# Kernel tuning notes

Hardware: AMD Instinct MI355X
Metric: run time of the kernel (lower is better)

## Reference

```python
import jax, jax.numpy as jnp
import numpy as np

IN, H, B = 1024, 1024, 8192


def _uniform(key, shape, stdv):
    return jax.random.uniform(key, shape, jnp.float32, -stdv, stdv)


def setup_inputs() -> dict:
    key = jax.random.key(0)
    ks = jax.random.split(key, 20)
    stdv = 1.0 / np.sqrt(H)
    inp = {
        "x": jax.random.normal(ks[0], (B, IN), jnp.float32),
        "h": jax.random.normal(ks[1], (B, H), jnp.float32),
        "c": jax.random.normal(ks[2], (B, H), jnp.float32),
        # fused input->gates weight [IN, 4H] (gate order: I, F, G, O) and bias [4H]
        "Wi": _uniform(ks[3], (IN, 4 * H), stdv),
        "bi": _uniform(ks[4], (4 * H,), stdv),
        # fused hidden->gates weight [H, 4H] and bias [4H]
        "Wh": _uniform(ks[5], (H, 4 * H), stdv),
        "bh": _uniform(ks[6], (4 * H,), stdv),
    }
    return inp


def reference(x, h, c, Wi, bi, Wh, bh):
    # Two fused GEMMs replacing the 8 separate nn.Linear calls (same math).
    gates = x @ Wi + bi + h @ Wh + bh  # [B, 4H]
    gI, gF, gG, gO = jnp.split(gates, 4, axis=-1)
    I = jax.nn.sigmoid(gI)
    F = jax.nn.sigmoid(gF)
    G = jnp.tanh(gG)   # nlF = Tanh
    O = jax.nn.sigmoid(gO)
    c_ = F * c + I * G
    h_ = O * jnp.tanh(c_)  # nlF2 = Tanh
    return (h_, c_)
```

## Files before the change

### kernel.cpp

```cpp
#include <hip/hip_runtime.h>
#include <stdint.h>

#define IN_DIM 1024
#define H_DIM  1024
#define BATCH  8192
#define KDIM   2048
#define NDIM   4096
#define BM     256
#define BN     256
#define BK     64
#define NT     (KDIM / BK)

typedef __bf16 bf16x8 __attribute__((ext_vector_type(8)));
typedef float  f32x4  __attribute__((ext_vector_type(4)));
typedef unsigned int u32;

static __device__ __forceinline__ unsigned short f2bf(float f) {
  u32 u = __builtin_bit_cast(u32, f);
  u += 0x7FFFu + ((u >> 16) & 1u);
  return (unsigned short)(u >> 16);
}

static __device__ __forceinline__ float sigm(float x) {
  return 1.0f / (1.0f + __expf(-x));
}
static __device__ __forceinline__ float tanh_fast(float x) {
  float e = __expf(-2.0f * fabsf(x));
  float t = (1.0f - e) / (1.0f + e);
  return copysignf(t, x);
}

__global__ void conv_a(const float* __restrict__ x, const float* __restrict__ h,
                       unsigned short* __restrict__ A) {
  const int total = BATCH * KDIM / 4;
  for (int i = blockIdx.x * blockDim.x + threadIdx.x; i < total;
       i += gridDim.x * blockDim.x) {
    int b = i >> 9;
    int k = (i & 511) << 2;
    const float* src = (k < IN_DIM) ? (x + (size_t)b * IN_DIM + k)
                                    : (h + (size_t)b * H_DIM + (k - IN_DIM));
    float4 v = *reinterpret_cast<const float4*>(src);
    ushort4 o;
    o.x = f2bf(v.x); o.y = f2bf(v.y); o.z = f2bf(v.z); o.w = f2bf(v.w);
    *reinterpret_cast<ushort4*>(A + (size_t)b * KDIM + k) = o;
  }
}

__global__ void conv_b(const float* __restrict__ Wi, const float* __restrict__ Wh,
                       unsigned short* __restrict__ Bt) {
  __shared__ float tile[32][33];
  int k0 = blockIdx.x * 32;
  int c0 = blockIdx.y * 32;
  int tx = threadIdx.x;
  int ty = threadIdx.y;
  const float* src = (k0 < IN_DIM) ? (Wi + (size_t)k0 * NDIM)
                                   : (Wh + (size_t)(k0 - IN_DIM) * NDIM);
  for (int i = 0; i < 4; i++) {
    int r = ty + 8 * i;
    tile[r][tx] = src[(size_t)r * NDIM + c0 + tx];
  }
  __syncthreads();
  int g = c0 >> 10;
  int ubase = c0 & 1023;
  for (int i = 0; i < 4; i++) {
    int cc = ty + 8 * i;
    int u = ubase + cc;
    int j = ((u >> 4) << 6) + (g << 4) + (u & 15);
    Bt[(size_t)j * KDIM + k0 + tx] = f2bf(tile[tx][cc]);
  }
}

__global__ void conv_bias(const float* __restrict__ bi, const float* __restrict__ bh,
                          float* __restrict__ bias) {
  int j = blockIdx.x * blockDim.x + threadIdx.x;
  if (j < NDIM) {
    int u = ((j >> 6) << 4) + (j & 15);
    int g = (j >> 4) & 3;
    int c = (g << 10) + u;
    bias[j] = bi[c] + bh[c];
  }
}

static __device__ __forceinline__ void gload_lds16(const void* g, void* l) {
  __builtin_amdgcn_global_load_lds(
      (const __attribute__((address_space(1))) u32*)g,
      (__attribute__((address_space(3))) u32*)l, 16, 0, 0);
}

#define MFMA __builtin_amdgcn_mfma_f32_16x16x32_bf16

__launch_bounds__(512, 2)
__global__ void lstm_gemm(const unsigned short* __restrict__ A,
                          const unsigned short* __restrict__ Bt,
                          const float* __restrict__ bias,
                          const float* __restrict__ Cin,
                          float* __restrict__ Hout,
                          float* __restrict__ Cout) {
  __shared__ __align__(16) char smem[131072];

  const int t  = threadIdx.x;
  const int l  = t & 63;
  const int w  = t >> 6;
  const int lane16 = l & 15;
  const int kg = l >> 4;
  const int wr = w >> 2;
  const int wc = w & 3;

  int bid = blockIdx.x;
  int swz = (bid & 7) * 64 + (bid >> 3);
  int brow = (swz >> 4) * BM;
  int bcol = (swz & 15) * BN;

  int slot0 = w * 128 + l, slot1 = slot0 + 64;
  int rih0 = slot0 >> 3, rih1 = slot1 >> 3;
  int c0 = (slot0 & 7) ^ (rih0 & 7), c1 = (slot1 & 7) ^ (rih1 & 7);

  const unsigned short* a0q0 = A + (size_t)(brow + (rih0 >> 6) * 128 + (rih0 & 63)) * KDIM + c0 * 8;
  const unsigned short* a0q1 = A + (size_t)(brow + (rih1 >> 6) * 128 + (rih1 & 63)) * KDIM + c1 * 8;
  const unsigned short* a1q0 = a0q0 + 131072;
  const unsigned short* a1q1 = a0q1 + 131072;
  const unsigned short* b0q0 = Bt + (size_t)(bcol + (rih0 >> 5) * 64 + (rih0 & 31)) * KDIM + c0 * 8;
  const unsigned short* b0q1 = Bt + (size_t)(bcol + (rih1 >> 5) * 64 + (rih1 & 31)) * KDIM + c1 * 8;
  const unsigned short* b1q0 = b0q0 + 65536;
  const unsigned short* b1q1 = b0q1 + 65536;

#define GL(gp, loff) gload_lds16((gp), smem + (loff) + w * 2048 + l * 16)

  const int msk = (lane16 & 7) << 4;
  char* vA0 = smem + wr * 8192 + lane16 * 128 + ((kg * 16) ^ msk);
  char* vA1 = smem + wr * 8192 + lane16 * 128 + ((64 + kg * 16) ^ msk);
  char* vB0 = smem + 65536 + wc * 4096 + lane16 * 128 + ((kg * 16) ^ msk);
  char* vB1 = smem + 65536 + wc * 4096 + lane16 * 128 + ((64 + kg * 16) ^ msk);

  f32x4 acc[8][4];
#pragma unroll
  for (int m = 0; m < 8; m++)
#pragma unroll
    for (int n = 0; n < 4; n++) acc[m][n] = (f32x4){0.f, 0.f, 0.f, 0.f};

  const int U = (bcol >> 2) + wc * 16 + lane16;
  const float* cinp = Cin + (size_t)(brow + wr * 128 + kg * 4) * H_DIM + U;
  float cin[32];
#pragma unroll
  for (int m = 0; m < 8; m++)
#pragma unroll
    for (int r = 0; r < 4; r++)
      cin[m * 4 + r] = cinp[(size_t)(m * 16 + r) * H_DIM];
  float bv[4];
#pragma unroll
  for (int nn = 0; nn < 4; nn++)
    bv[nn] = bias[bcol + wc * 64 + nn * 16 + lane16];

  GL(a0q0, 0);                 GL(a0q1, 1024);
  GL(b0q0, 65536);             GL(b0q1, 65536 + 1024);
  GL(a1q0, 16384);             GL(a1q1, 16384 + 1024);
  GL(b1q0, 65536 + 16384);     GL(b1q1, 65536 + 16384 + 1024);
  GL(a0q0 + 64, 32768);        GL(a0q1 + 64, 32768 + 1024);
  GL(b0q0 + 64, 65536 + 32768);GL(b0q1 + 64, 65536 + 32768 + 1024);
  GL(a1q0 + 64, 32768 + 16384);GL(a1q1 + 64, 32768 + 16384 + 1024);
  asm volatile("s_waitcnt vmcnt(6)" ::: "memory");
  __builtin_amdgcn_s_barrier();
  a0q0 += 128; a0q1 += 128; a1q0 += 128; a1q1 += 128;
  b0q0 += 128; b0q1 += 128; b1q0 += 64;  b1q1 += 64;

  bf16x8 afr[4][2], bfr[4][2];

#define BODY(P)                                                              \
  {                                                                          \
    \
    _Pragma("unroll") for (int mm = 0; mm < 4; mm++) {                       \
      afr[mm][0] = *(const bf16x8*)(vA0 + (P)*32768 + mm*2048);              \
      afr[mm][1] = *(const bf16x8*)(vA1 + (P)*32768 + mm*2048);              \
    }                                                                        \
    _Pragma("unroll") for (int nn = 0; nn < 2; nn++) {                       \
      bfr[nn][0] = *(const bf16x8*)(vB0 + (P)*32768 + nn*2048);              \
      bfr[nn][1] = *(const bf16x8*)(vB1 + (P)*32768 + nn*2048);              \
    }                                                                        \
    GL(b1q0, 65536 + ((P)^1)*32768 + 16384);                                 \
    GL(b1q1, 65536 + ((P)^1)*32768 + 16384 + 1024);                          \
    __builtin_amdgcn_s_barrier();                                            \
    asm volatile("s_waitcnt lgkmcnt(0)" ::: "memory");                       \
    __builtin_amdgcn_s_setprio(1);                                           \
    _Pragma("unroll") for (int mm = 0; mm < 4; mm++)                         \
      _Pragma("unroll") for (int nn = 0; nn < 2; nn++) {                     \
        acc[mm][nn] = MFMA(afr[mm][0], bfr[nn][0], acc[mm][nn], 0, 0, 0);    \
        acc[mm][nn] = MFMA(afr[mm][1], bfr[nn][1], acc[mm][nn], 0, 0, 0);    \
      }                                                                      \
    __builtin_amdgcn_s_setprio(0);                                           \
    __builtin_amdgcn_s_barrier();                                            \
                     \
    _Pragma("unroll") for (int nn = 2; nn < 4; nn++) {                       \
      bfr[nn][0] = *(const bf16x8*)(vB0 + (P)*32768 + 16384 + (nn-2)*2048);  \
      bfr[nn][1] = *(const bf16x8*)(vB1 + (P)*32768 + 16384 + (nn-2)*2048);  \
    }                                                                        \
    GL(a0q0, (P)*32768);                                                     \
    GL(a0q1, (P)*32768 + 1024);                                              \
    __builtin_amdgcn_s_barrier();                                            \
    asm volatile("s_waitcnt lgkmcnt(0)" ::: "memory");                       \
    __builtin_amdgcn_s_setprio(1);                                           \
    _Pragma("unroll") for (int mm = 0; mm < 4; mm++)                         \
      _Pragma("unroll") for (int nn = 2; nn < 4; nn++) {                     \
        acc[mm][nn] = MFMA(afr[mm][0], bfr[nn][0], acc[mm][nn], 0, 0, 0);    \
        acc[mm][nn] = MFMA(afr[mm][1], bfr[nn][1], acc[mm][nn], 0, 0, 0);    \
      }                                                                      \
    __builtin_amdgcn_s_setprio(0);                                           \
    __builtin_amdgcn_s_barrier();                                            \
                     \
    _Pragma("unroll") for (int mm = 0; mm < 4; mm++) {                       \
      afr[mm][0] = *(const bf16x8*)(vA0 + (P)*32768 + 16384 + mm*2048);      \
      afr[mm][1] = *(const bf16x8*)(vA1 + (P)*32768 + 16384 + mm*2048);      \
    }                                                                        \
    GL(b0q0, 65536 + (P)*32768);                                             \
    GL(b0q1, 65536 + (P)*32768 + 1024);                                      \
    __builtin_amdgcn_s_barrier();                                            \
    asm volatile("s_waitcnt lgkmcnt(0)" ::: "memory");                       \
    __builtin_amdgcn_s_setprio(1);                                           \
    _Pragma("unroll") for (int mm = 0; mm < 4; mm++)                         \
      _Pragma("unroll") for (int nn = 0; nn < 2; nn++) {                     \
        acc[4+mm][nn] = MFMA(afr[mm][0], bfr[nn][0], acc[4+mm][nn], 0, 0, 0);\
        acc[4+mm][nn] = MFMA(afr[mm][1], bfr[nn][1], acc[4+mm][nn], 0, 0, 0);\
      }                                                                      \
    __builtin_amdgcn_s_setprio(0);                                           \
    __builtin_amdgcn_s_barrier();                                            \
       \
    GL(a1q0, (P)*32768 + 16384);                                             \
    GL(a1q1, (P)*32768 + 16384 + 1024);                                      \
    asm volatile("s_waitcnt vmcnt(6)" ::: "memory");                         \
    __builtin_amdgcn_s_barrier();                                            \
    __builtin_amdgcn_s_setprio(1);                                           \
    _Pragma("unroll") for (int mm = 0; mm < 4; mm++)                         \
      _Pragma("unroll") for (int nn = 2; nn < 4; nn++) {                     \
        acc[4+mm][nn] = MFMA(afr[mm][0], bfr[nn][0], acc[4+mm][nn], 0, 0, 0);\
        acc[4+mm][nn] = MFMA(afr[mm][1], bfr[nn][1], acc[4+mm][nn], 0, 0, 0);\
      }                                                                      \
    __builtin_amdgcn_s_setprio(0);                                           \
    __builtin_amdgcn_s_barrier();                                            \
    a0q0 += 64; a0q1 += 64; a1q0 += 64; a1q1 += 64;                          \
    b0q0 += 64; b0q1 += 64; b1q0 += 64; b1q1 += 64;                          \
  }

  for (int it = 0; it < NT / 2; ++it) {
    BODY(0)
    BODY(1)
  }
#undef BODY
#undef GL

  float* hp = Hout + (size_t)(brow + wr * 128 + kg * 4) * H_DIM + U;
  float* cp = Cout + (size_t)(brow + wr * 128 + kg * 4) * H_DIM + U;
#pragma unroll
  for (int m = 0; m < 8; m++)
#pragma unroll
    for (int r = 0; r < 4; r++) {
      float Ig = sigm(acc[m][0][r] + bv[0]);
      float Fg = sigm(acc[m][1][r] + bv[1]);
      float Gg = tanh_fast(acc[m][2][r] + bv[2]);
      float Og = sigm(acc[m][3][r] + bv[3]);
      float cn = Fg * cin[m * 4 + r] + Ig * Gg;
      size_t off = (size_t)(m * 16 + r) * H_DIM;
      hp[off] = Og * tanh_fast(cn);
      cp[off] = cn;
    }

  asm volatile("s_waitcnt vmcnt(0)" ::: "memory");
}

extern "C" void kernel_launch(void* const* d_in, const int* in_sizes, int n_in,
                              void* d_out, int out_size, void* d_ws, size_t ws_size,
                              hipStream_t stream) {
  const float* x  = (const float*)d_in[0];
  const float* h  = (const float*)d_in[1];
  const float* c  = (const float*)d_in[2];
  const float* Wi = (const float*)d_in[3];
  const float* bi = (const float*)d_in[4];
  const float* Wh = (const float*)d_in[5];
  const float* bh = (const float*)d_in[6];

  float* out  = (float*)d_out;
  float* Hout = out;
  float* Cout = out + (size_t)BATCH * H_DIM;

  unsigned short* Abf = (unsigned short*)d_ws;
  unsigned short* Btb = (unsigned short*)((char*)d_ws + 33554432);
  float*          bsf = (float*)((char*)d_ws + 50331648);

  conv_a<<<2048, 256, 0, stream>>>(x, h, Abf);
  conv_b<<<dim3(64, 128), dim3(32, 8), 0, stream>>>(Wi, Wh, Btb);
  conv_bias<<<16, 256, 0, stream>>>(bi, bh, bsf);
  lstm_gemm<<<512, 512, 0, stream>>>(Abf, Btb, bsf, c, Hout, Cout);
}
```

Before: 178.6 us.

## Double-buffer A fragments and prefetch next stage's LDS reads across MFMA blocks

Splits the A register fragments into two sets so the next half-tile's A and first B fragments are read from LDS while the current MFMA block is still running. The explicit lgkmcnt(0) waits go away, leaving the compiler to insert the waits. The c-input and bias loads move from before the main loop to the epilogue, which frees 36 registers during the K loop. The cost is more live fragment registers and exposed global-load latency for c in the epilogue.

```diff
diff --git a/kernel.cpp b/kernel.cpp
--- a/kernel.cpp
+++ b/kernel.cpp
@@ -138,19 +138,6 @@
 #pragma unroll
     for (int n = 0; n < 4; n++) acc[m][n] = (f32x4){0.f, 0.f, 0.f, 0.f};
 
-  const int U = (bcol >> 2) + wc * 16 + lane16;
-  const float* cinp = Cin + (size_t)(brow + wr * 128 + kg * 4) * H_DIM + U;
-  float cin[32];
-#pragma unroll
-  for (int m = 0; m < 8; m++)
-#pragma unroll
-    for (int r = 0; r < 4; r++)
-      cin[m * 4 + r] = cinp[(size_t)(m * 16 + r) * H_DIM];
-  float bv[4];
-#pragma unroll
-  for (int nn = 0; nn < 4; nn++)
-    bv[nn] = bias[bcol + wc * 64 + nn * 16 + lane16];
-
   GL(a0q0, 0);                 GL(a0q1, 1024);
   GL(b0q0, 65536);             GL(b0q1, 65536 + 1024);
   GL(a1q0, 16384);             GL(a1q1, 16384 + 1024);
@@ -163,75 +150,84 @@
   a0q0 += 128; a0q1 += 128; a1q0 += 128; a1q1 += 128;
   b0q0 += 128; b0q1 += 128; b1q0 += 64;  b1q1 += 64;
 
-  bf16x8 afr[4][2], bfr[4][2];
+  bf16x8 afrA[4][2], afrB[4][2], bfr[4][2];
+
+#pragma unroll
+  for (int mm = 0; mm < 4; mm++) {
+    afrA[mm][0] = *(const bf16x8*)(vA0 + mm * 2048);
+    afrA[mm][1] = *(const bf16x8*)(vA1 + mm * 2048);
+  }
+#pragma unroll
+  for (int nn = 0; nn < 2; nn++) {
+    bfr[nn][0] = *(const bf16x8*)(vB0 + nn * 2048);
+    bfr[nn][1] = *(const bf16x8*)(vB1 + nn * 2048);
+  }
 
 #define BODY(P)                                                              \
   {                                                                          \
-    \
-    _Pragma("unroll") for (int mm = 0; mm < 4; mm++) {                       \
-      afr[mm][0] = *(const bf16x8*)(vA0 + (P)*32768 + mm*2048);              \
-      afr[mm][1] = *(const bf16x8*)(vA1 + (P)*32768 + mm*2048);              \
-    }                                                                        \
-    _Pragma("unroll") for (int nn = 0; nn < 2; nn++) {                       \
-      bfr[nn][0] = *(const bf16x8*)(vB0 + (P)*32768 + nn*2048);              \
-      bfr[nn][1] = *(const bf16x8*)(vB1 + (P)*32768 + nn*2048);              \
-    }                                                                        \
-    GL(b1q0, 65536 + ((P)^1)*32768 + 16384);                                 \
-    GL(b1q1, 65536 + ((P)^1)*32768 + 16384 + 1024);                          \
-    __builtin_amdgcn_s_barrier();                                            \
-    asm volatile("s_waitcnt lgkmcnt(0)" ::: "memory");                       \
-    __builtin_amdgcn_s_setprio(1);                                           \
-    _Pragma("unroll") for (int mm = 0; mm < 4; mm++)                         \
-      _Pragma("unroll") for (int nn = 0; nn < 2; nn++) {                     \
-        acc[mm][nn] = MFMA(afr[mm][0], bfr[nn][0], acc[mm][nn], 0, 0, 0);    \
-        acc[mm][nn] = MFMA(afr[mm][1], bfr[nn][1], acc[mm][nn], 0, 0, 0);    \
-      }                                                                      \
-    __builtin_amdgcn_s_setprio(0);                                           \
-    __builtin_amdgcn_s_barrier();                                            \
-                     \
+      \
     _Pragma("unroll") for (int nn = 2; nn < 4; nn++) {                       \
       bfr[nn][0] = *(const bf16x8*)(vB0 + (P)*32768 + 16384 + (nn-2)*2048);  \
       bfr[nn][1] = *(const bf16x8*)(vB1 + (P)*32768 + 16384 + (nn-2)*2048);  \
     }                                                                        \
+    GL(b1q0, 65536 + ((P)^1)*32768 + 16384);                                 \
+    GL(b1q1, 65536 + ((P)^1)*32768 + 16384 + 1024);                          \
+    __builtin_amdgcn_s_barrier();                                            \
+    __builtin_amdgcn_s_setprio(1);                                           \
+    _Pragma("unroll") for (int mm = 0; mm < 4; mm++)                         \
+      _Pragma("unroll") for (int nn = 0; nn < 2; nn++) {                     \
+        acc[mm][nn] = MFMA(afrA[mm][0], bfr[nn][0], acc[mm][nn], 0, 0, 0);   \
+        acc[mm][nn] = MFMA(afrA[mm][1], bfr[nn][1], acc[mm][nn], 0, 0, 0);   \
+      }                                                                      \
+    __builtin_amdgcn_s_setprio(0);                                           \
+    __builtin_amdgcn_s_barrier();                                            \
+       \
+    _Pragma("unroll") for (int mm = 0; mm < 4; mm++) {                       \
+      afrB[mm][0] = *(const bf16x8*)(vA0 + (P)*32768 + 16384 + mm*2048);     \
+      afrB[mm][1] = *(const bf16x8*)(vA1 + (P)*32768 + 16384 + mm*2048);     \
+    }                                                                        \
     GL(a0q0, (P)*32768);                                                     \
     GL(a0q1, (P)*32768 + 1024);                                              \
     __builtin_amdgcn_s_barrier();                                            \
-    asm volatile("s_waitcnt lgkmcnt(0)" ::: "memory");                       \
     __builtin_amdgcn_s_setprio(1);                                           \
     _Pragma("unroll") for (int mm = 0; mm < 4; mm++)                         \
       _Pragma("unroll") for (int nn = 2; nn < 4; nn++) {                     \
-        acc[mm][nn] = MFMA(afr[mm][0], bfr[nn][0], acc[mm][nn], 0, 0, 0);    \
-        acc[mm][nn] = MFMA(afr[mm][1], bfr[nn][1], acc[mm][nn], 0, 0, 0);    \
+        acc[mm][nn] = MFMA(afrA[mm][0], bfr[nn][0], acc[mm][nn], 0, 0, 0);   \
+        acc[mm][nn] = MFMA(afrA[mm][1], bfr[nn][1], acc[mm][nn], 0, 0, 0);   \
       }                                                                      \
     __builtin_amdgcn_s_setprio(0);                                           \
     __builtin_amdgcn_s_barrier();                                            \
-                     \
-    _Pragma("unroll") for (int mm = 0; mm < 4; mm++) {                       \
-      afr[mm][0] = *(const bf16x8*)(vA0 + (P)*32768 + 16384 + mm*2048);      \
-      afr[mm][1] = *(const bf16x8*)(vA1 + (P)*32768 + 16384 + mm*2048);      \
-    }                                                                        \
+                         \
     GL(b0q0, 65536 + (P)*32768);                                             \
     GL(b0q1, 65536 + (P)*32768 + 1024);                                      \
     __builtin_amdgcn_s_barrier();                                            \
-    asm volatile("s_waitcnt lgkmcnt(0)" ::: "memory");                       \
     __builtin_amdgcn_s_setprio(1);                                           \
     _Pragma("unroll") for (int mm = 0; mm < 4; mm++)                         \
       _Pragma("unroll") for (int nn = 0; nn < 2; nn++) {                     \
-        acc[4+mm][nn] = MFMA(afr[mm][0], bfr[nn][0], acc[4+mm][nn], 0, 0, 0);\
-        acc[4+mm][nn] = MFMA(afr[mm][1], bfr[nn][1], acc[4+mm][nn], 0, 0, 0);\
+        acc[4+mm][nn] = MFMA(afrB[mm][0], bfr[nn][0], acc[4+mm][nn], 0, 0, 0);\
+        acc[4+mm][nn] = MFMA(afrB[mm][1], bfr[nn][1], acc[4+mm][nn], 0, 0, 0);\
       }                                                                      \
     __builtin_amdgcn_s_setprio(0);                                           \
     __builtin_amdgcn_s_barrier();                                            \
-       \
+                                            \
     GL(a1q0, (P)*32768 + 16384);                                             \
     GL(a1q1, (P)*32768 + 16384 + 1024);                                      \
     asm volatile("s_waitcnt vmcnt(6)" ::: "memory");                         \
     __builtin_amdgcn_s_barrier();                                            \
+    __builtin_amdgcn_sched_barrier(0);  \
+    _Pragma("unroll") for (int mm = 0; mm < 4; mm++) {                       \
+      afrA[mm][0] = *(const bf16x8*)(vA0 + ((P)^1)*32768 + mm*2048);         \
+      afrA[mm][1] = *(const bf16x8*)(vA1 + ((P)^1)*32768 + mm*2048);         \
+    }                                                                        \
+    _Pragma("unroll") for (int nn = 0; nn < 2; nn++) {                       \
+      bfr[nn][0] = *(const bf16x8*)(vB0 + ((P)^1)*32768 + nn*2048);          \
+      bfr[nn][1] = *(const bf16x8*)(vB1 + ((P)^1)*32768 + nn*2048);          \
+    }                                                                        \
     __builtin_amdgcn_s_setprio(1);                                           \
     _Pragma("unroll") for (int mm = 0; mm < 4; mm++)                         \
       _Pragma("unroll") for (int nn = 2; nn < 4; nn++) {                     \
-        acc[4+mm][nn] = MFMA(afr[mm][0], bfr[nn][0], acc[4+mm][nn], 0, 0, 0);\
-        acc[4+mm][nn] = MFMA(afr[mm][1], bfr[nn][1], acc[4+mm][nn], 0, 0, 0);\
+        acc[4+mm][nn] = MFMA(afrB[mm][0], bfr[nn][0], acc[4+mm][nn], 0, 0, 0);\
+        acc[4+mm][nn] = MFMA(afrB[mm][1], bfr[nn][1], acc[4+mm][nn], 0, 0, 0);\
       }                                                                      \
     __builtin_amdgcn_s_setprio(0);                                           \
     __builtin_amdgcn_s_barrier();                                            \
@@ -245,6 +241,21 @@
   }
 #undef BODY
 #undef GL
+
+  asm volatile("s_waitcnt vmcnt(0)" ::: "memory");
+
+  const int U = (bcol >> 2) + wc * 16 + lane16;
+  const float* cinp = Cin + (size_t)(brow + wr * 128 + kg * 4) * H_DIM + U;
+  float cin[32];
+#pragma unroll
+  for (int m = 0; m < 8; m++)
+#pragma unroll
+    for (int r = 0; r < 4; r++)
+      cin[m * 4 + r] = cinp[(size_t)(m * 16 + r) * H_DIM];
+  float bv[4];
+#pragma unroll
+  for (int nn = 0; nn < 4; nn++)
+    bv[nn] = bias[bcol + wc * 64 + nn * 16 + lane16];
 
   float* hp = Hout + (size_t)(brow + wr * 128 + kg * 4) * H_DIM + U;
   float* cp = Cout + (size_t)(brow + wr * 128 + kg * 4) * H_DIM + U;
@@ -261,8 +272,6 @@
       hp[off] = Og * tanh_fast(cn);
       cp[off] = cn;
     }
-
-  asm volatile("s_waitcnt vmcnt(0)" ::: "memory");
 }
 
 extern "C" void kernel_launch(void* const* d_in, const int* in_sizes, int n_in,
```

Result: slower. 202.5 us (+13.4%).
